# Kernel optimization log

Measured on AMD Instinct MI355X. Metric: run time of the kernel, lower is better.

## Reference

```python
import jax, jax.numpy as jnp
import numpy as np

N_NODES = 100000
N_EDGES = 1600000
D_IN = 64
D_OUT = 64


def setup_inputs() -> dict:
    key = jax.random.key(0)
    k1, k2, k3, k4, k5, k6, k7 = jax.random.split(key, 7)
    x = jax.random.normal(k1, (N_NODES, D_IN), dtype=jnp.float32)
    edge_index = jax.random.randint(k2, (2, N_EDGES), 0, N_NODES, dtype=jnp.int64)
    pos_encoding = jax.random.normal(k3, (N_NODES, D_IN), dtype=jnp.float32)
    # GCNConv linear weight (no bias inside lin; bias added post-aggregation)
    W_gcn = jax.random.normal(k4, (D_IN, D_OUT), dtype=jnp.float32) / np.sqrt(D_IN)
    b_gcn = jax.random.normal(k5, (D_OUT,), dtype=jnp.float32) * 0.01
    # positional encoding Linear
    W_pos = jax.random.normal(k6, (D_IN, D_OUT), dtype=jnp.float32) / np.sqrt(D_IN)
    b_pos = jax.random.normal(k7, (D_OUT,), dtype=jnp.float32) * 0.01
    return {"x": x, "edge_index": edge_index, "pos_encoding": pos_encoding,
            "W_gcn": W_gcn, "b_gcn": b_gcn, "W_pos": W_pos, "b_pos": b_pos}


def _gcn_conv(x, edge_index, W, b):
    n = x.shape[0]
    # add self-loops (PyG GCNConv default)
    loop = jnp.arange(n, dtype=edge_index.dtype)
    src = jnp.concatenate([edge_index[0], loop])
    dst = jnp.concatenate([edge_index[1], loop])
    # symmetric normalization: deg over destination with unit edge weights
    deg = jax.ops.segment_sum(jnp.ones_like(src, dtype=x.dtype), dst, num_segments=n)
    dinv = jnp.where(deg > 0, jax.lax.rsqrt(deg), 0.0)
    norm = dinv[src] * dinv[dst]  # [E+N]
    h = x @ W  # [N, D_OUT]
    msg = h[src] * norm[:, None]  # gather + scale
    out = jax.ops.segment_sum(msg, dst, num_segments=n)  # scatter-add
    return out + b


def reference(x, edge_index, pos_encoding, W_gcn, b_gcn, W_pos, b_pos):
    conv_out = _gcn_conv(x, edge_index, W_gcn, b_gcn)
    pos = pos_encoding @ W_pos + b_pos
    return conv_out + pos
```

## Files before the change

kernel.cpp:

```cpp
#include <hip/hip_runtime.h>
#include <hip/hip_fp16.h>

#define NN 100000
#define NE 1600000
#define D  64

#define SB    256
#define CHUNK 6250
#define BSH   7
#define BMSK  127
#define NB    782
#define PAD   784
#define CAPS  2560
#define GPD   68

typedef __attribute__((ext_vector_type(8))) _Float16 f16x8;
typedef __attribute__((ext_vector_type(4))) float    f32x4;

__device__ __forceinline__ void scan_bsum_wave0(const int* __restrict__ bsum,
                                                int* binoff_l, int t) {
    if (t < 64) {
        int base = t * 13;
        int loc[13]; int run = 0;
#pragma unroll
        for (int j = 0; j < 13; ++j) {
            int idx = base + j;
            int v = (idx < NB) ? bsum[idx] : 0;
            loc[j] = run; run += v;
        }
        int pre = run;
#pragma unroll
        for (int off = 1; off < 64; off <<= 1) {
            int u = __shfl_up(pre, off);
            if (t >= off) pre += u;
        }
        pre -= run;
#pragma unroll
        for (int j = 0; j < 13; ++j) {
            int idx = base + j;
            if (idx <= NB) binoff_l[idx] = pre + loc[j];
        }
    }
}

__global__ __launch_bounds__(1024) void k_hist(const int* __restrict__ dst,
                                               int* __restrict__ hist) {
    __shared__ int h[NB];
    int t = threadIdx.x, blk = blockIdx.x;
    for (int i = t; i < NB; i += 1024) h[i] = 0;
    __syncthreads();
    int e0 = blk * CHUNK;
    for (int e = e0 + t; e < e0 + CHUNK; e += 1024)
        atomicAdd(&h[dst[e] >> BSH], 1);
    __syncthreads();
    for (int i = t; i < NB; i += 1024) hist[blk * PAD + i] = h[i];
}

__global__ __launch_bounds__(1024) void k_scanT(int* __restrict__ hist,
                                                int* __restrict__ bsum) {
    __shared__ int ps[256][33];
    int t = threadIdx.x, b0 = blockIdx.x * 32;
    for (int i = t; i < 256 * 32; i += 1024) {
        int r = i >> 5, cc = i & 31;
        int bin = b0 + cc;
        ps[r][cc] = (bin < NB) ? hist[r * PAD + bin] : 0;
    }
    __syncthreads();
    int w = t >> 6, lane = t & 63;
    for (int cc = w; cc < 32; cc += 16) {
        int base = lane * 4;
        int v0 = ps[base][cc], v1 = ps[base + 1][cc];
        int v2 = ps[base + 2][cc], v3 = ps[base + 3][cc];
        int run = v0 + v1 + v2 + v3;
        int pre = run;
#pragma unroll
        for (int off = 1; off < 64; off <<= 1) {
            int u = __shfl_up(pre, off);
            if (lane >= off) pre += u;
        }
        pre -= run;
        ps[base][cc]     = pre;
        ps[base + 1][cc] = pre + v0;
        ps[base + 2][cc] = pre + v0 + v1;
        ps[base + 3][cc] = pre + v0 + v1 + v2;
        if (lane == 63 && b0 + cc < NB) bsum[b0 + cc] = pre + run;
    }
    __syncthreads();
    for (int i = t; i < 256 * 32; i += 1024) {
        int r = i >> 5, cc = i & 31;
        int bin = b0 + cc;
        if (bin < NB) hist[r * PAD + bin] = ps[r][cc];
    }
}

__global__ __launch_bounds__(1024) void k_scatter1(
    const int* __restrict__ src, const int* __restrict__ dst,
    const int* __restrict__ hist, const int* __restrict__ bsum,
    unsigned* __restrict__ ebuf)
{
    __shared__ int cur[NB];
    __shared__ int binoff_l[NB + 1];
    int t = threadIdx.x, blk = blockIdx.x;
    scan_bsum_wave0(bsum, binoff_l, t);
    __syncthreads();
    for (int i = t; i < NB; i += 1024)
        cur[i] = binoff_l[i] + hist[blk * PAD + i];
    __syncthreads();
    int e0 = blk * CHUNK;
    for (int e = e0 + t; e < e0 + CHUNK; e += 1024) {
        int d = dst[e];
        int p = atomicAdd(&cur[d >> BSH], 1);
        ebuf[p] = ((unsigned)src[e] << BSH) | (unsigned)(d & BMSK);
    }
}

__global__ __launch_bounds__(512) void k_count(const int* __restrict__ bsum,
                                               const unsigned* __restrict__ ebuf,
                                               float* __restrict__ dinv) {
    __shared__ int c[128];
    __shared__ int binoff_l[NB + 1];
    int t = threadIdx.x, b = blockIdx.x;
    scan_bsum_wave0(bsum, binoff_l, t);
    if (t < 128) c[t] = 0;
    __syncthreads();
    int e0 = binoff_l[b], e1 = binoff_l[b + 1];
    for (int e = e0 + t; e < e1; e += 512)
        atomicAdd(&c[ebuf[e] & BMSK], 1);
    __syncthreads();
    if (t < 128) {
        int node = (b << BSH) + t;
        if (node < NN) dinv[node] = rsqrtf((float)(c[t] + 1));
    }
}

__global__ __launch_bounds__(256) void k_mm(
    const float* __restrict__ x, const float* __restrict__ Wg,
    const float* __restrict__ dinv, __half* __restrict__ g)
{
    __shared__ __align__(16) _Float16 Wt[64][64];
    int t = threadIdx.x;
    int lane = t & 63;
    int wid = t >> 6;

    if (blockIdx.x == 0 && t < 64) g[(long)NN * D + t] = __float2half(0.f);

    for (int i = t; i < 64 * 64; i += 256) {
        int k = i >> 6, n = i & 63;
        Wt[n][k] = (_Float16)Wg[i];
    }
    __syncthreads();

    int lr = lane & 15, lg = lane >> 4;
    int kofs = lg * 8;

    f16x8 b[4][2];
#pragma unroll
    for (int n = 0; n < 4; ++n)
#pragma unroll
        for (int kt = 0; kt < 2; ++kt)
            b[n][kt] = *(const f16x8*)&Wt[n * 16 + lr][kt * 32 + kofs];

    for (int rb0 = blockIdx.x * 64; rb0 < NN; rb0 += gridDim.x * 64) {
        int rb = rb0 + wid * 16;
        int arow = rb + lr;
        int arc = arow < NN ? arow : NN - 1;
        const float4* ap = (const float4*)(x + (long)arc * 64 + kofs);
        float4 p0 = ap[0], p1 = ap[1], p2 = ap[8], p3 = ap[9];
        f16x8 a0, a1;
        a0[0] = (_Float16)p0.x; a0[1] = (_Float16)p0.y;
        a0[2] = (_Float16)p0.z; a0[3] = (_Float16)p0.w;
        a0[4] = (_Float16)p1.x; a0[5] = (_Float16)p1.y;
        a0[6] = (_Float16)p1.z; a0[7] = (_Float16)p1.w;
        a1[0] = (_Float16)p2.x; a1[1] = (_Float16)p2.y;
        a1[2] = (_Float16)p2.z; a1[3] = (_Float16)p2.w;
        a1[4] = (_Float16)p3.x; a1[5] = (_Float16)p3.y;
        a1[6] = (_Float16)p3.z; a1[7] = (_Float16)p3.w;

        f32x4 z = {0.f, 0.f, 0.f, 0.f};
        f32x4 acc[4] = {z, z, z, z};
#pragma unroll
        for (int n = 0; n < 4; ++n) {
            acc[n] = __builtin_amdgcn_mfma_f32_16x16x32_f16(a0, b[n][0], acc[n], 0, 0, 0);
            acc[n] = __builtin_amdgcn_mfma_f32_16x16x32_f16(a1, b[n][1], acc[n], 0, 0, 0);
        }

        int orow0 = rb + lg * 4;
#pragma unroll
        for (int r = 0; r < 4; ++r) {
            int row = orow0 + r;
            if (row < NN) {
                float di = dinv[row];
#pragma unroll
                for (int n = 0; n < 4; ++n)
                    g[(long)row * D + n * 16 + lr] = __float2half(acc[n][r] * di);
            }
        }
    }
}

__global__ __launch_bounds__(512) void k_gather(
    const int* __restrict__ bsum, unsigned* __restrict__ ebuf,
    const __half* __restrict__ g,
    const float* __restrict__ pos, const float* __restrict__ Wp,
    const float* __restrict__ bg, const float* __restrict__ bp,
    float* __restrict__ out)
{
    __shared__ unsigned cache[CAPS];
    __shared__ float gres[128 * GPD];
    __shared__ __align__(16) _Float16 Wt[64][64];
    __shared__ int c[128];
    __shared__ int cur[128];
    __shared__ int rs_l[129];
    __shared__ int binoff_l[NB + 1];
    int t = threadIdx.x, b = blockIdx.x;
    int lane = t & 63, w = t >> 6;

    for (int i = t; i < 64 * 64; i += 512) {
        int k = i >> 6, n = i & 63;
        Wt[n][k] = (_Float16)Wp[i];
    }
    scan_bsum_wave0(bsum, binoff_l, t);
    if (t < 128) c[t] = 0;
    __syncthreads();
    int e0 = binoff_l[b];
    int cnt = binoff_l[b + 1] - e0;

    for (int i = t; i < cnt; i += 512) {
        unsigned u = ebuf[e0 + i];
        if (i < CAPS) cache[i] = u;
        atomicAdd(&c[u & BMSK], 1);
    }
    __syncthreads();

    if (t < 64) {
        int l0 = c[2 * t], l1 = c[2 * t + 1];
        int run = l0 + l1;
        int pre = run;
#pragma unroll
        for (int off = 1; off < 64; off <<= 1) {
            int u = __shfl_up(pre, off);
            if (t >= off) pre += u;
        }
        pre -= run;
        rs_l[2 * t] = pre;          cur[2 * t] = pre;
        rs_l[2 * t + 1] = pre + l0; cur[2 * t + 1] = pre + l0;
        if (t == 63) rs_l[128] = pre + run;
    }

    unsigned ur[8]; int nmy = 0;
    for (int i = t, j = 0; i < cnt && j < 8; i += 512, ++j) {
        ur[j] = (i < CAPS) ? cache[i] : ebuf[e0 + i];
        nmy = j + 1;
    }
    __syncthreads();
    for (int j = 0; j < nmy; ++j) {
        unsigned u = ur[j];
        int p = atomicAdd(&cur[u & BMSK], 1);
        unsigned s = u >> BSH;
        if (p < CAPS) cache[p] = s; else ebuf[e0 + p] = s;
    }
    __syncthreads();

    int f = lane & 7;
    int grp = lane >> 3;
    const uint4* gq = (const uint4*)g;
    for (int p = 0; p < 16; ++p) {
        int r = p * 8 + w;
        int node = (b << BSH) + r;
        if (node >= NN) continue;
        int rs0 = rs_l[r];
        int nl = rs_l[r + 1] - rs0;
        float a0 = 0.f, a1 = 0.f, a2 = 0.f, a3 = 0.f;
        float a4 = 0.f, a5 = 0.f, a6 = 0.f, a7 = 0.f;
        int NG = (nl + 7) >> 3;
        for (int c2 = 0; c2 < NG; ++c2) {
            int idx = c2 * 8 + grp;
            int s = NN;
            if (idx < nl) {
                int ii = rs0 + idx;
                s = (ii < CAPS) ? (int)cache[ii] : (int)ebuf[e0 + ii];
            }
            uint4 u = gq[(long)s * 8 + f];
            __half2 h0 = *(__half2*)&u.x, h1 = *(__half2*)&u.y;
            __half2 h2 = *(__half2*)&u.z, h3 = *(__half2*)&u.w;
            a0 += __low2float(h0); a1 += __high2float(h0);
            a2 += __low2float(h1); a3 += __high2float(h1);
            a4 += __low2float(h2); a5 += __high2float(h2);
            a6 += __low2float(h3); a7 += __high2float(h3);
        }
#pragma unroll
        for (int mask = 8; mask <= 32; mask <<= 1) {
            a0 += __shfl_xor(a0, mask); a1 += __shfl_xor(a1, mask);
            a2 += __shfl_xor(a2, mask); a3 += __shfl_xor(a3, mask);
            a4 += __shfl_xor(a4, mask); a5 += __shfl_xor(a5, mask);
            a6 += __shfl_xor(a6, mask); a7 += __shfl_xor(a7, mask);
        }
        if (lane < 16) {
            int ff = lane & 7, hs = lane >> 3;
            uint4 u = gq[(long)node * 8 + ff];
            __half2 s0 = hs ? *(__half2*)&u.z : *(__half2*)&u.x;
            __half2 s1 = hs ? *(__half2*)&u.w : *(__half2*)&u.y;
            float b0 = hs ? a4 : a0, b1 = hs ? a5 : a1;
            float b2 = hs ? a6 : a2, b3 = hs ? a7 : a3;
            float di = rsqrtf((float)(c[r] + 1));
            float4 o;
            o.x = (b0 + __low2float(s0)) * di;
            o.y = (b1 + __high2float(s0)) * di;
            o.z = (b2 + __low2float(s1)) * di;
            o.w = (b3 + __high2float(s1)) * di;
            *(float4*)&gres[r * GPD + (ff * 2 + hs) * 4] = o;
        }
    }
    __syncthreads();

    int lr = lane & 15, lg = lane >> 4;
    int kofs = lg * 8;
    f16x8 bfr[4][2];
#pragma unroll
    for (int n = 0; n < 4; ++n)
#pragma unroll
        for (int kt = 0; kt < 2; ++kt)
            bfr[n][kt] = *(const f16x8*)&Wt[n * 16 + lr][kt * 32 + kofs];
    float bias[4];
#pragma unroll
    for (int n = 0; n < 4; ++n) {
        int cc = n * 16 + lr;
        bias[n] = bg[cc] + bp[cc];
    }
    int node0 = (b << BSH);
    int rb = w * 16;
    int arow = node0 + rb + lr;
    int arc = arow < NN ? arow : NN - 1;
    const float4* ap = (const float4*)(pos + (long)arc * 64 + kofs);
    float4 p0 = ap[0], p1 = ap[1], p2 = ap[8], p3 = ap[9];
    f16x8 a0, a1;
    a0[0] = (_Float16)p0.x; a0[1] = (_Float16)p0.y;
    a0[2] = (_Float16)p0.z; a0[3] = (_Float16)p0.w;
    a0[4] = (_Float16)p1.x; a0[5] = (_Float16)p1.y;
    a0[6] = (_Float16)p1.z; a0[7] = (_Float16)p1.w;
    a1[0] = (_Float16)p2.x; a1[1] = (_Float16)p2.y;
    a1[2] = (_Float16)p2.z; a1[3] = (_Float16)p2.w;
    a1[4] = (_Float16)p3.x; a1[5] = (_Float16)p3.y;
    a1[6] = (_Float16)p3.z; a1[7] = (_Float16)p3.w;
    f32x4 z = {0.f, 0.f, 0.f, 0.f};
    f32x4 acc[4] = {z, z, z, z};
#pragma unroll
    for (int n = 0; n < 4; ++n) {
        acc[n] = __builtin_amdgcn_mfma_f32_16x16x32_f16(a0, bfr[n][0], acc[n], 0, 0, 0);
        acc[n] = __builtin_amdgcn_mfma_f32_16x16x32_f16(a1, bfr[n][1], acc[n], 0, 0, 0);
    }
    int orow0 = rb + lg * 4;
#pragma unroll
    for (int r = 0; r < 4; ++r) {
        int row = orow0 + r;
        int node = node0 + row;
        if (node < NN) {
#pragma unroll
            for (int n = 0; n < 4; ++n)
                out[(long)node * 64 + n * 16 + lr] =
                    acc[n][r] + bias[n] + gres[row * GPD + n * 16 + lr];
        }
    }
}

extern "C" void kernel_launch(void* const* d_in, const int* in_sizes, int n_in,
                              void* d_out, int out_size, void* d_ws, size_t ws_size,
                              hipStream_t stream) {
    const float* x   = (const float*)d_in[0];
    const int*   ei  = (const int*)d_in[1];
    const float* pos = (const float*)d_in[2];
    const float* Wg  = (const float*)d_in[3];
    const float* bg  = (const float*)d_in[4];
    const float* Wp  = (const float*)d_in[5];
    const float* bp  = (const float*)d_in[6];
    float* out = (float*)d_out;

    const int* src = ei;
    const int* dst = ei + NE;

    char* Wb = (char*)d_ws;
    unsigned* ebuf = (unsigned*)Wb;
    __half*   g    = (__half*)(Wb + 6400000);
    int*      hist = (int*)(Wb + 19200128);
    int*      bsum = hist + SB * PAD;
    float*    dinv = (float*)(bsum + 784);

    hipLaunchKernelGGL(k_hist,     dim3(SB),   dim3(1024), 0, stream, dst, hist);
    hipLaunchKernelGGL(k_scanT,    dim3(25),   dim3(1024), 0, stream, hist, bsum);
    hipLaunchKernelGGL(k_scatter1, dim3(SB),   dim3(1024), 0, stream,
                       src, dst, hist, bsum, ebuf);
    hipLaunchKernelGGL(k_count,    dim3(NB),   dim3(512),  0, stream,
                       bsum, ebuf, dinv);
    hipLaunchKernelGGL(k_mm,       dim3(1024), dim3(256),  0, stream,
                       x, Wg, dinv, g);
    hipLaunchKernelGGL(k_gather,   dim3(NB),   dim3(512),  0, stream,
                       bsum, ebuf, g, pos, Wp, bg, bp, out);
}
```

Before: 220.6 us.

## Co-schedule pos matmul with histogram and x matmul with degree count

Moves the positional-encoding matmul out of the gather kernel and into a combined launch with the histogram kernel, writing bias plus pos projection straight to out. The x@W matmul now runs in the same launch as the degree count and no longer depends on dinv. The source-side dinv scaling moves into the gather loop as an extra per-edge load and FMA, and the gather does a read-modify-write on out. The aim is to overlap independent work, cut a launch, and shrink the gather's shared memory (no gres/Wt) to raise occupancy. The cost is extra per-edge dinv loads and extra out traffic.

```diff
diff --git a/kernel.cpp b/kernel.cpp
--- a/kernel.cpp
+++ b/kernel.cpp
@@ -12,7 +12,6 @@
 #define NB    782
 #define PAD   784
 #define CAPS  2560
-#define GPD   68
 
 typedef __attribute__((ext_vector_type(8))) _Float16 f16x8;
 typedef __attribute__((ext_vector_type(4))) float    f32x4;
@@ -43,128 +42,55 @@
     }
 }
 
-__global__ __launch_bounds__(1024) void k_hist(const int* __restrict__ dst,
-                                               int* __restrict__ hist) {
-    __shared__ int h[NB];
-    int t = threadIdx.x, blk = blockIdx.x;
-    for (int i = t; i < NB; i += 1024) h[i] = 0;
-    __syncthreads();
-    int e0 = blk * CHUNK;
-    for (int e = e0 + t; e < e0 + CHUNK; e += 1024)
-        atomicAdd(&h[dst[e] >> BSH], 1);
-    __syncthreads();
-    for (int i = t; i < NB; i += 1024) hist[blk * PAD + i] = h[i];
-}
-
-__global__ __launch_bounds__(1024) void k_scanT(int* __restrict__ hist,
-                                                int* __restrict__ bsum) {
-    __shared__ int ps[256][33];
-    int t = threadIdx.x, b0 = blockIdx.x * 32;
-    for (int i = t; i < 256 * 32; i += 1024) {
-        int r = i >> 5, cc = i & 31;
-        int bin = b0 + cc;
-        ps[r][cc] = (bin < NB) ? hist[r * PAD + bin] : 0;
-    }
-    __syncthreads();
-    int w = t >> 6, lane = t & 63;
-    for (int cc = w; cc < 32; cc += 16) {
-        int base = lane * 4;
-        int v0 = ps[base][cc], v1 = ps[base + 1][cc];
-        int v2 = ps[base + 2][cc], v3 = ps[base + 3][cc];
-        int run = v0 + v1 + v2 + v3;
-        int pre = run;
-#pragma unroll
-        for (int off = 1; off < 64; off <<= 1) {
-            int u = __shfl_up(pre, off);
-            if (lane >= off) pre += u;
-        }
-        pre -= run;
-        ps[base][cc]     = pre;
-        ps[base + 1][cc] = pre + v0;
-        ps[base + 2][cc] = pre + v0 + v1;
-        ps[base + 3][cc] = pre + v0 + v1 + v2;
-        if (lane == 63 && b0 + cc < NB) bsum[b0 + cc] = pre + run;
-    }
-    __syncthreads();
-    for (int i = t; i < 256 * 32; i += 1024) {
-        int r = i >> 5, cc = i & 31;
-        int bin = b0 + cc;
-        if (bin < NB) hist[r * PAD + bin] = ps[r][cc];
-    }
-}
-
-__global__ __launch_bounds__(1024) void k_scatter1(
-    const int* __restrict__ src, const int* __restrict__ dst,
-    const int* __restrict__ hist, const int* __restrict__ bsum,
-    unsigned* __restrict__ ebuf)
+__global__ __launch_bounds__(256) void k_mm2hist(
+    const float* __restrict__ pos, const float* __restrict__ Wp,
+    const float* __restrict__ bg, const float* __restrict__ bp,
+    float* __restrict__ out,
+    const int* __restrict__ dst, int* __restrict__ hist)
 {
-    __shared__ int cur[NB];
-    __shared__ int binoff_l[NB + 1];
-    int t = threadIdx.x, blk = blockIdx.x;
-    scan_bsum_wave0(bsum, binoff_l, t);
-    __syncthreads();
-    for (int i = t; i < NB; i += 1024)
-        cur[i] = binoff_l[i] + hist[blk * PAD + i];
-    __syncthreads();
-    int e0 = blk * CHUNK;
-    for (int e = e0 + t; e < e0 + CHUNK; e += 1024) {
-        int d = dst[e];
-        int p = atomicAdd(&cur[d >> BSH], 1);
-        ebuf[p] = ((unsigned)src[e] << BSH) | (unsigned)(d & BMSK);
-    }
-}
-
-__global__ __launch_bounds__(512) void k_count(const int* __restrict__ bsum,
-                                               const unsigned* __restrict__ ebuf,
-                                               float* __restrict__ dinv) {
-    __shared__ int c[128];
-    __shared__ int binoff_l[NB + 1];
-    int t = threadIdx.x, b = blockIdx.x;
-    scan_bsum_wave0(bsum, binoff_l, t);
-    if (t < 128) c[t] = 0;
-    __syncthreads();
-    int e0 = binoff_l[b], e1 = binoff_l[b + 1];
-    for (int e = e0 + t; e < e1; e += 512)
-        atomicAdd(&c[ebuf[e] & BMSK], 1);
-    __syncthreads();
-    if (t < 128) {
-        int node = (b << BSH) + t;
-        if (node < NN) dinv[node] = rsqrtf((float)(c[t] + 1));
-    }
-}
-
-__global__ __launch_bounds__(256) void k_mm(
-    const float* __restrict__ x, const float* __restrict__ Wg,
-    const float* __restrict__ dinv, __half* __restrict__ g)
-{
-    __shared__ __align__(16) _Float16 Wt[64][64];
+    __shared__ union {
+        __align__(16) _Float16 Wt[64][64];
+        int h[NB];
+    } sm;
     int t = threadIdx.x;
-    int lane = t & 63;
-    int wid = t >> 6;
-
-    if (blockIdx.x == 0 && t < 64) g[(long)NN * D + t] = __float2half(0.f);
-
+
+    if (blockIdx.x >= 782) {
+        int blk = blockIdx.x - 782;
+        for (int i = t; i < NB; i += 256) sm.h[i] = 0;
+        __syncthreads();
+        int e0 = blk * CHUNK;
+        for (int e = e0 + t; e < e0 + CHUNK; e += 256)
+            atomicAdd(&sm.h[dst[e] >> BSH], 1);
+        __syncthreads();
+        for (int i = t; i < NB; i += 256) hist[blk * PAD + i] = sm.h[i];
+        return;
+    }
+
+    int lane = t & 63, wid = t >> 6;
     for (int i = t; i < 64 * 64; i += 256) {
         int k = i >> 6, n = i & 63;
-        Wt[n][k] = (_Float16)Wg[i];
-    }
-    __syncthreads();
-
+        sm.Wt[n][k] = (_Float16)Wp[i];
+    }
+    __syncthreads();
     int lr = lane & 15, lg = lane >> 4;
     int kofs = lg * 8;
-
     f16x8 b[4][2];
 #pragma unroll
     for (int n = 0; n < 4; ++n)
 #pragma unroll
         for (int kt = 0; kt < 2; ++kt)
-            b[n][kt] = *(const f16x8*)&Wt[n * 16 + lr][kt * 32 + kofs];
-
-    for (int rb0 = blockIdx.x * 64; rb0 < NN; rb0 += gridDim.x * 64) {
+            b[n][kt] = *(const f16x8*)&sm.Wt[n * 16 + lr][kt * 32 + kofs];
+    float bsv[4];
+#pragma unroll
+    for (int n = 0; n < 4; ++n) {
+        int cc = n * 16 + lr;
+        bsv[n] = bg[cc] + bp[cc];
+    }
+    for (int rb0 = blockIdx.x * 64; rb0 < NN; rb0 += 782 * 64) {
         int rb = rb0 + wid * 16;
         int arow = rb + lr;
         int arc = arow < NN ? arow : NN - 1;
-        const float4* ap = (const float4*)(x + (long)arc * 64 + kofs);
+        const float4* ap = (const float4*)(pos + (long)arc * 64 + kofs);
         float4 p0 = ap[0], p1 = ap[1], p2 = ap[8], p3 = ap[9];
         f16x8 a0, a1;
         a0[0] = (_Float16)p0.x; a0[1] = (_Float16)p0.y;
@@ -175,7 +101,6 @@
         a1[2] = (_Float16)p2.z; a1[3] = (_Float16)p2.w;
         a1[4] = (_Float16)p3.x; a1[5] = (_Float16)p3.y;
         a1[6] = (_Float16)p3.z; a1[7] = (_Float16)p3.w;
-
         f32x4 z = {0.f, 0.f, 0.f, 0.f};
         f32x4 acc[4] = {z, z, z, z};
 #pragma unroll
@@ -183,31 +108,162 @@
             acc[n] = __builtin_amdgcn_mfma_f32_16x16x32_f16(a0, b[n][0], acc[n], 0, 0, 0);
             acc[n] = __builtin_amdgcn_mfma_f32_16x16x32_f16(a1, b[n][1], acc[n], 0, 0, 0);
         }
-
         int orow0 = rb + lg * 4;
 #pragma unroll
         for (int r = 0; r < 4; ++r) {
             int row = orow0 + r;
             if (row < NN) {
-                float di = dinv[row];
 #pragma unroll
                 for (int n = 0; n < 4; ++n)
-                    g[(long)row * D + n * 16 + lr] = __float2half(acc[n][r] * di);
+                    out[(long)row * 64 + n * 16 + lr] = acc[n][r] + bsv[n];
             }
+        }
+    }
+}
+
+__global__ __launch_bounds__(1024) void k_scanT(int* __restrict__ hist,
+                                                int* __restrict__ bsum) {
+    __shared__ int ps[256][33];
+    int t = threadIdx.x, b0 = blockIdx.x * 32;
+    for (int i = t; i < 256 * 32; i += 1024) {
+        int r = i >> 5, cc = i & 31;
+        int bin = b0 + cc;
+        ps[r][cc] = (bin < NB) ? hist[r * PAD + bin] : 0;
+    }
+    __syncthreads();
+    int w = t >> 6, lane = t & 63;
+    for (int cc = w; cc < 32; cc += 16) {
+        int base = lane * 4;
+        int v0 = ps[base][cc], v1 = ps[base + 1][cc];
+        int v2 = ps[base + 2][cc], v3 = ps[base + 3][cc];
+        int run = v0 + v1 + v2 + v3;
+        int pre = run;
+#pragma unroll
+        for (int off = 1; off < 64; off <<= 1) {
+            int u = __shfl_up(pre, off);
+            if (lane >= off) pre += u;
+        }
+        pre -= run;
+        ps[base][cc]     = pre;
+        ps[base + 1][cc] = pre + v0;
+        ps[base + 2][cc] = pre + v0 + v1;
+        ps[base + 3][cc] = pre + v0 + v1 + v2;
+        if (lane == 63 && b0 + cc < NB) bsum[b0 + cc] = pre + run;
+    }
+    __syncthreads();
+    for (int i = t; i < 256 * 32; i += 1024) {
+        int r = i >> 5, cc = i & 31;
+        int bin = b0 + cc;
+        if (bin < NB) hist[r * PAD + bin] = ps[r][cc];
+    }
+}
+
+__global__ __launch_bounds__(1024) void k_scatter1(
+    const int* __restrict__ src, const int* __restrict__ dst,
+    const int* __restrict__ hist, const int* __restrict__ bsum,
+    unsigned* __restrict__ ebuf)
+{
+    __shared__ int cur[NB];
+    __shared__ int binoff_l[NB + 1];
+    int t = threadIdx.x, blk = blockIdx.x;
+    scan_bsum_wave0(bsum, binoff_l, t);
+    __syncthreads();
+    for (int i = t; i < NB; i += 1024)
+        cur[i] = binoff_l[i] + hist[blk * PAD + i];
+    __syncthreads();
+    int e0 = blk * CHUNK;
+    for (int e = e0 + t; e < e0 + CHUNK; e += 1024) {
+        int d = dst[e];
+        int p = atomicAdd(&cur[d >> BSH], 1);
+        ebuf[p] = ((unsigned)src[e] << BSH) | (unsigned)(d & BMSK);
+    }
+}
+
+__global__ __launch_bounds__(512) void k_countmm1(
+    const int* __restrict__ bsum, const unsigned* __restrict__ ebuf,
+    float* __restrict__ dinv,
+    const float* __restrict__ x, const float* __restrict__ Wg,
+    __half* __restrict__ g)
+{
+    __shared__ union {
+        struct { int c[128]; int binoff_l[NB + 1]; } cs;
+        __align__(16) _Float16 Wt[64][64];
+    } sm;
+    int t = threadIdx.x;
+
+    if (blockIdx.x < 782) {
+        int b = blockIdx.x;
+        scan_bsum_wave0(bsum, sm.cs.binoff_l, t);
+        if (t < 128) sm.cs.c[t] = 0;
+        __syncthreads();
+        int e0 = sm.cs.binoff_l[b], e1 = sm.cs.binoff_l[b + 1];
+        for (int e = e0 + t; e < e1; e += 512)
+            atomicAdd(&sm.cs.c[ebuf[e] & BMSK], 1);
+        __syncthreads();
+        if (t < 128) {
+            int node = (b << BSH) + t;
+            if (node < NN) dinv[node] = rsqrtf((float)(sm.cs.c[t] + 1));
+            else if (node == NN) dinv[node] = 0.f;
+        }
+        return;
+    }
+
+    int blk = blockIdx.x - 782;
+    int lane = t & 63, wid = t >> 6;
+    if (blk == 0 && t < 64) g[(long)NN * D + t] = __float2half(0.f);
+    for (int i = t; i < 64 * 64; i += 512) {
+        int k = i >> 6, n = i & 63;
+        sm.Wt[n][k] = (_Float16)Wg[i];
+    }
+    __syncthreads();
+    int lr = lane & 15, lg = lane >> 4;
+    int kofs = lg * 8;
+    f16x8 b[4][2];
+#pragma unroll
+    for (int n = 0; n < 4; ++n)
+#pragma unroll
+        for (int kt = 0; kt < 2; ++kt)
+            b[n][kt] = *(const f16x8*)&sm.Wt[n * 16 + lr][kt * 32 + kofs];
+
+    int rb = blk * 128 + wid * 16;
+    int arow = rb + lr;
+    int arc = arow < NN ? arow : NN - 1;
+    const float4* ap = (const float4*)(x + (long)arc * 64 + kofs);
+    float4 p0 = ap[0], p1 = ap[1], p2 = ap[8], p3 = ap[9];
+    f16x8 a0, a1;
+    a0[0] = (_Float16)p0.x; a0[1] = (_Float16)p0.y;
+    a0[2] = (_Float16)p0.z; a0[3] = (_Float16)p0.w;
+    a0[4] = (_Float16)p1.x; a0[5] = (_Float16)p1.y;
+    a0[6] = (_Float16)p1.z; a0[7] = (_Float16)p1.w;
+    a1[0] = (_Float16)p2.x; a1[1] = (_Float16)p2.y;
+    a1[2] = (_Float16)p2.z; a1[3] = (_Float16)p2.w;
+    a1[4] = (_Float16)p3.x; a1[5] = (_Float16)p3.y;
+    a1[6] = (_Float16)p3.z; a1[7] = (_Float16)p3.w;
+    f32x4 z = {0.f, 0.f, 0.f, 0.f};
+    f32x4 acc[4] = {z, z, z, z};
+#pragma unroll
+    for (int n = 0; n < 4; ++n) {
+        acc[n] = __builtin_amdgcn_mfma_f32_16x16x32_f16(a0, b[n][0], acc[n], 0, 0, 0);
+        acc[n] = __builtin_amdgcn_mfma_f32_16x16x32_f16(a1, b[n][1], acc[n], 0, 0, 0);
+    }
+    int orow0 = rb + lg * 4;
+#pragma unroll
+    for (int r = 0; r < 4; ++r) {
+        int row = orow0 + r;
+        if (row < NN) {
+#pragma unroll
+            for (int n = 0; n < 4; ++n)
+                g[(long)row * D + n * 16 + lr] = __float2half(acc[n][r]);
         }
     }
 }
 
 __global__ __launch_bounds__(512) void k_gather(
     const int* __restrict__ bsum, unsigned* __restrict__ ebuf,
-    const __half* __restrict__ g,
-    const float* __restrict__ pos, const float* __restrict__ Wp,
-    const float* __restrict__ bg, const float* __restrict__ bp,
+    const float* __restrict__ dinv, const __half* __restrict__ g,
     float* __restrict__ out)
 {
     __shared__ unsigned cache[CAPS];
-    __shared__ float gres[128 * GPD];
-    __shared__ __align__(16) _Float16 Wt[64][64];
     __shared__ int c[128];
     __shared__ int cur[128];
     __shared__ int rs_l[129];
@@ -215,10 +271,6 @@
     int t = threadIdx.x, b = blockIdx.x;
     int lane = t & 63, w = t >> 6;
 
-    for (int i = t; i < 64 * 64; i += 512) {
-        int k = i >> 6, n = i & 63;
-        Wt[n][k] = (_Float16)Wp[i];
-    }
     scan_bsum_wave0(bsum, binoff_l, t);
     if (t < 128) c[t] = 0;
     __syncthreads();
@@ -273,6 +325,7 @@
         float a0 = 0.f, a1 = 0.f, a2 = 0.f, a3 = 0.f;
         float a4 = 0.f, a5 = 0.f, a6 = 0.f, a7 = 0.f;
         int NG = (nl + 7) >> 3;
+#pragma unroll 2
         for (int c2 = 0; c2 < NG; ++c2) {
             int idx = c2 * 8 + grp;
             int s = NN;
@@ -281,12 +334,13 @@
                 s = (ii < CAPS) ? (int)cache[ii] : (int)ebuf[e0 + ii];
             }
             uint4 u = gq[(long)s * 8 + f];
+            float ds = dinv[s];
             __half2 h0 = *(__half2*)&u.x, h1 = *(__half2*)&u.y;
             __half2 h2 = *(__half2*)&u.z, h3 = *(__half2*)&u.w;
-            a0 += __low2float(h0); a1 += __high2float(h0);
-            a2 += __low2float(h1); a3 += __high2float(h1);
-            a4 += __low2float(h2); a5 += __high2float(h2);
-            a6 += __low2float(h3); a7 += __high2float(h3);
+            a0 = fmaf(ds, __low2float(h0), a0); a1 = fmaf(ds, __high2float(h0), a1);
+            a2 = fmaf(ds, __low2float(h1), a2); a3 = fmaf(ds, __high2float(h1), a3);
+            a4 = fmaf(ds, __low2float(h2), a4); a5 = fmaf(ds, __high2float(h2), a5);
+            a6 = fmaf(ds, __low2float(h3), a6); a7 = fmaf(ds, __high2float(h3), a7);
         }
 #pragma unroll
         for (int mask = 8; mask <= 32; mask <<= 1) {
@@ -303,62 +357,13 @@
             float b0 = hs ? a4 : a0, b1 = hs ? a5 : a1;
             float b2 = hs ? a6 : a2, b3 = hs ? a7 : a3;
             float di = rsqrtf((float)(c[r] + 1));
-            float4 o;
-            o.x = (b0 + __low2float(s0)) * di;
-            o.y = (b1 + __high2float(s0)) * di;
-            o.z = (b2 + __low2float(s1)) * di;
-            o.w = (b3 + __high2float(s1)) * di;
-            *(float4*)&gres[r * GPD + (ff * 2 + hs) * 4] = o;
-        }
-    }
-    __syncthreads();
-
-    int lr = lane & 15, lg = lane >> 4;
-    int kofs = lg * 8;
-    f16x8 bfr[4][2];
-#pragma unroll
-    for (int n = 0; n < 4; ++n)
-#pragma unroll
-        for (int kt = 0; kt < 2; ++kt)
-            bfr[n][kt] = *(const f16x8*)&Wt[n * 16 + lr][kt * 32 + kofs];
-    float bias[4];
-#pragma unroll
-    for (int n = 0; n < 4; ++n) {
-        int cc = n * 16 + lr;
-        bias[n] = bg[cc] + bp[cc];
-    }
-    int node0 = (b << BSH);
-    int rb = w * 16;
-    int arow = node0 + rb + lr;
-    int arc = arow < NN ? arow : NN - 1;
-    const float4* ap = (const float4*)(pos + (long)arc * 64 + kofs);
-    float4 p0 = ap[0], p1 = ap[1], p2 = ap[8], p3 = ap[9];
-    f16x8 a0, a1;
-    a0[0] = (_Float16)p0.x; a0[1] = (_Float16)p0.y;
-    a0[2] = (_Float16)p0.z; a0[3] = (_Float16)p0.w;
-    a0[4] = (_Float16)p1.x; a0[5] = (_Float16)p1.y;
-    a0[6] = (_Float16)p1.z; a0[7] = (_Float16)p1.w;
-    a1[0] = (_Float16)p2.x; a1[1] = (_Float16)p2.y;
-    a1[2] = (_Float16)p2.z; a1[3] = (_Float16)p2.w;
-    a1[4] = (_Float16)p3.x; a1[5] = (_Float16)p3.y;
-    a1[6] = (_Float16)p3.z; a1[7] = (_Float16)p3.w;
-    f32x4 z = {0.f, 0.f, 0.f, 0.f};
-    f32x4 acc[4] = {z, z, z, z};
-#pragma unroll
-    for (int n = 0; n < 4; ++n) {
-        acc[n] = __builtin_amdgcn_mfma_f32_16x16x32_f16(a0, bfr[n][0], acc[n], 0, 0, 0);
-        acc[n] = __builtin_amdgcn_mfma_f32_16x16x32_f16(a1, bfr[n][1], acc[n], 0, 0, 0);
-    }
-    int orow0 = rb + lg * 4;
-#pragma unroll
-    for (int r = 0; r < 4; ++r) {
-        int row = orow0 + r;
-        int node = node0 + row;
-        if (node < NN) {
-#pragma unroll
-            for (int n = 0; n < 4; ++n)
-                out[(long)node * 64 + n * 16 + lr] =
-                    acc[n][r] + bias[n] + gres[row * GPD + n * 16 + lr];
+            float4* op = (float4*)(out + (long)node * D) + (ff * 2 + hs);
+            float4 o = *op;
+            o.x += (b0 + di * __low2float(s0)) * di;
+            o.y += (b1 + di * __high2float(s0)) * di;
+            o.z += (b2 + di * __low2float(s1)) * di;
+            o.w += (b3 + di * __high2float(s1)) * di;
+            *op = o;
         }
     }
 }
@@ -385,14 +390,13 @@
     int*      bsum = hist + SB * PAD;
     float*    dinv = (float*)(bsum + 784);
 
-    hipLaunchKernelGGL(k_hist,     dim3(SB),   dim3(1024), 0, stream, dst, hist);
+    hipLaunchKernelGGL(k_mm2hist,  dim3(1038), dim3(256),  0, stream,
+                       pos, Wp, bg, bp, out, dst, hist);
     hipLaunchKernelGGL(k_scanT,    dim3(25),   dim3(1024), 0, stream, hist, bsum);
     hipLaunchKernelGGL(k_scatter1, dim3(SB),   dim3(1024), 0, stream,
                        src, dst, hist, bsum, ebuf);
-    hipLaunchKernelGGL(k_count,    dim3(NB),   dim3(512),  0, stream,
-                       bsum, ebuf, dinv);
-    hipLaunchKernelGGL(k_mm,       dim3(1024), dim3(256),  0, stream,
-                       x, Wg, dinv, g);
+    hipLaunchKernelGGL(k_countmm1, dim3(1564), dim3(512),  0, stream,
+                       bsum, ebuf, dinv, x, Wg, g);
     hipLaunchKernelGGL(k_gather,   dim3(NB),   dim3(512),  0, stream,
-                       bsum, ebuf, g, pos, Wp, bg, bp, out);
-}
+                       bsum, ebuf, dinv, g, out);
+}
```

Result: faster. 214.0 us (-3.0%).
